# Optimization experiments

Hardware: AMD Instinct MI355X
Metric: run time of the kernel (lower is better)

The kernel has to match this reference:

```python
import jax, jax.numpy as jnp
import numpy as np

N = 100000   # nodes
E = 1600000  # edges (avg degree 16)
D = 64       # input feature dim


def _lin(k, i, o):
    return (jax.random.normal(k, (i, o), jnp.float32) / np.float32(np.sqrt(i)))


def setup_inputs() -> dict:
    key = jax.random.key(0)
    ks = jax.random.split(key, 12)
    return {
        "x": jax.random.normal(ks[0], (N, D), jnp.float32),
        "edge_index": jax.random.randint(ks[1], (2, E), 0, N, dtype=jnp.int64),
        # layer 1: SAGEConv(64, 64, 'pool')
        "W1_pool": _lin(ks[2], 64, 64), "b1_pool": jnp.zeros((64,), jnp.float32),
        "W1_self": _lin(ks[3], 64, 64), "W1_neigh": _lin(ks[4], 64, 64),
        "b1": jnp.zeros((64,), jnp.float32),
        # layer 2: SAGEConv(64, 32, 'pool')
        "W2_pool": _lin(ks[5], 64, 64), "b2_pool": jnp.zeros((64,), jnp.float32),
        "W2_self": _lin(ks[6], 64, 32), "W2_neigh": _lin(ks[7], 64, 32),
        "b2": jnp.zeros((32,), jnp.float32),
        # layer 3: SAGEConv(32, 32, 'mean')
        "W3_self": _lin(ks[8], 32, 32), "W3_neigh": _lin(ks[9], 32, 32),
        "b3": jnp.zeros((32,), jnp.float32),
    }


def _sage_pool(x, src, dst, Wp, bp, Ws, Wn, b):
    # max-pool aggregator: transform all nodes once (cheaper than per-edge),
    # gather per-edge, segment-max into destination nodes.
    m = jax.nn.relu(x @ Wp + bp)[src]                      # [E, in]
    agg = jax.ops.segment_max(m, dst, num_segments=N)     # [N, in]
    agg = jnp.where(jnp.isfinite(agg), agg, jnp.float32(0.0))  # isolated nodes -> 0
    return x @ Ws + agg @ Wn + b


def _sage_mean(x, src, dst, Ws, Wn, b):
    s = jax.ops.segment_sum(x[src], dst, num_segments=N)   # [N, in]
    cnt = jax.ops.segment_sum(jnp.ones((src.shape[0],), jnp.float32), dst,
                              num_segments=N)
    agg = s / jnp.maximum(cnt, jnp.float32(1.0))[:, None]
    return x @ Ws + agg @ Wn + b


def reference(x, edge_index,
              W1_pool, b1_pool, W1_self, W1_neigh, b1,
              W2_pool, b2_pool, W2_self, W2_neigh, b2,
              W3_self, W3_neigh, b3):
    src, dst = edge_index[0], edge_index[1]
    h = jax.nn.relu(_sage_pool(x, src, dst, W1_pool, b1_pool, W1_self, W1_neigh, b1))
    h = _sage_pool(h, src, dst, W2_pool, b2_pool, W2_self, W2_neigh, b2)
    h = _sage_mean(h, src, dst, W3_self, W3_neigh, b3)
    return h
```

## Files before the change

### kernel.cpp

```cpp
#include <hip/hip_runtime.h>
#include <hip/hip_bf16.h>


typedef unsigned int uint;
typedef short short8 __attribute__((ext_vector_type(8)));
typedef float f32x4 __attribute__((ext_vector_type(4)));
typedef float f32x2 __attribute__((ext_vector_type(2)));
typedef unsigned short u16x8 __attribute__((ext_vector_type(8)));

__device__ __forceinline__ float bf2f(unsigned short h){
  return __uint_as_float(((uint)h) << 16);
}
__device__ __forceinline__ unsigned short f2bf(float f){
  uint u = __float_as_uint(f);
  u += 0x7fffu + ((u >> 16) & 1u);
  return (unsigned short)(u >> 16);
}
__device__ __forceinline__ float lo16(uint u){ return __uint_as_float(u << 16); }
__device__ __forceinline__ float hi16(uint u){ return __uint_as_float(u & 0xffff0000u); }

__device__ __forceinline__ uint4 pkmax4(uint4 a, uint4 b){
  u16x8 x = __builtin_bit_cast(u16x8, a);
  u16x8 y = __builtin_bit_cast(u16x8, b);
  return __builtin_bit_cast(uint4, __builtin_elementwise_max(x, y));
}
__device__ __forceinline__ uint4 shflx4(uint4 a, int off){
  uint4 r;
  r.x = (uint)__shfl_xor((int)a.x, off, 64);
  r.y = (uint)__shfl_xor((int)a.y, off, 64);
  r.z = (uint)__shfl_xor((int)a.z, off, 64);
  r.w = (uint)__shfl_xor((int)a.w, off, 64);
  return r;
}
__device__ __forceinline__ f32x2 b2lo(uint u){
  f32x2 r; r.x = lo16(u); r.y = hi16(u); return r;
}

struct WConv {
  const void* src[13];
  int n[13], isbias[13], Cs[13], K[13], off[13];
};

__global__ void conv_w(WConv wc, unsigned short* wtbase, float* bbase,
                       const unsigned short* x, const int* ei,
                       int* flags, int* ccur, int NB){
  __shared__ int sflags[2];
  int t = threadIdx.x;
  if (t < 64){
    int sane = 0;
    #pragma unroll
    for (int k = 0; k < 4; ++k){
      int e = (x[(t * 4 + k) * 2] >> 7) & 0xff;
      sane += (e >= 118 && e <= 134);
    }
    #pragma unroll
    for (int off = 32; off; off >>= 1) sane += __shfl_down(sane, off, 64);
    unsigned long long b = __ballot(ei[1 + 2 * t] != 0);
    if (t == 0){ sflags[0] = (sane >= 128); sflags[1] = (b == 0ull); }
  }
  __syncthreads();
  int isbf = sflags[0];
  if (blockIdx.x == 0){
    if (t == 0){ flags[0] = sflags[0]; flags[1] = sflags[1]; }
    for (int i = t; i < NB; i += 256) ccur[i] = 0;
  }
  int bt = blockIdx.x, n = wc.n[bt];
  if (wc.isbias[bt]){
    float* d = bbase + wc.off[bt];
    for (int i = t; i < n; i += 256)
      d[i] = isbf ? bf2f(((const unsigned short*)wc.src[bt])[i])
                  : ((const float*)wc.src[bt])[i];
  } else {
    unsigned short* d = wtbase + wc.off[bt];
    int Cs = wc.Cs[bt], K = wc.K[bt], Cm = (1 << Cs) - 1;
    for (int i = t; i < n; i += 256){
      int k = i >> Cs, c = i & Cm;
      unsigned short v = isbf ? ((const unsigned short*)wc.src[bt])[i]
                              : f2bf(((const float*)wc.src[bt])[i]);
      d[c * K + k] = v;
    }
  }
}

__device__ __forceinline__ void load_edge(const void* ei, int E, int is64, int e,
                                          int& s, int& d){
  if (is64){
    const long long* p = (const long long*)ei;
    s = (int)p[e]; d = (int)p[E + e];
  } else {
    const int* p = (const int*)ei;
    s = p[e]; d = p[E + e];
  }
}

#define CSR_CE 8192

__global__ __launch_bounds__(256) void csr_phase1(
    const void* __restrict__ ei, const int* __restrict__ flags,
    int* __restrict__ ccur, uint* __restrict__ pairs,
    int E, int N, int NB, int S, int CAP)
{
  __shared__ uint hist[1024];
  __shared__ uint gbase[1024];
  int is64 = flags[1];
  int t = threadIdx.x;
  uint dmask = (1u << S) - 1u;
  int e0 = blockIdx.x * CSR_CE;
  for (int i = t; i < 1024; i += 256) hist[i] = 0;
  __syncthreads();
  #pragma unroll 4
  for (int it = 0; it < CSR_CE / 256; ++it){
    int e = e0 + it * 256 + t;
    if (e >= E) break;
    int s, d; load_edge(ei, E, is64, e, s, d);
    if ((unsigned)s >= (unsigned)N || (unsigned)d >= (unsigned)N) continue;
    atomicAdd(&hist[d >> S], 1u);
  }
  __syncthreads();
  for (int b = t; b < NB; b += 256){
    uint c = hist[b];
    if (c) gbase[b] = (uint)atomicAdd(&ccur[b], (int)c);
    hist[b] = 0;
  }
  __syncthreads();
  #pragma unroll 4
  for (int it = 0; it < CSR_CE / 256; ++it){
    int e = e0 + it * 256 + t;
    if (e >= E) break;
    int s, d; load_edge(ei, E, is64, e, s, d);
    if ((unsigned)s >= (unsigned)N || (unsigned)d >= (unsigned)N) continue;
    int b = d >> S;
    uint local = atomicAdd(&hist[b], 1u);
    uint pos = gbase[b] + local;
    if (pos >= (uint)CAP) pos = (uint)CAP - 1;
    pairs[(size_t)b * CAP + pos] = ((uint)s << S) | ((uint)d & dmask);
  }
}

__global__ void csr_scan0(const int* __restrict__ ccur, int* __restrict__ cbase,
                          int* __restrict__ rowptrN, int NB, int CAP)
{
  __shared__ int sm[256];
  int t = threadIdx.x;
  int g = (NB + 255) / 256;
  int vb = t * g, v[4], s = 0;
  for (int k = 0; k < g; ++k){
    int i = vb + k; int x = (i < NB) ? min(ccur[i], CAP) : 0; v[k] = x; s += x;
  }
  sm[t] = s; __syncthreads();
  for (int off = 1; off < 256; off <<= 1){
    int x = (t >= off) ? sm[t - off] : 0;
    __syncthreads(); sm[t] += x; __syncthreads();
  }
  int run = sm[t] - s;
  for (int k = 0; k < g; ++k){
    int i = vb + k;
    if (i < NB){ cbase[i] = run; run += v[k]; }
  }
  if (t == 255){ cbase[NB] = run; *rowptrN = run; }
}

#define P2_CAP 6144
__global__ __launch_bounds__(256) void csr_phase2(
    const int* __restrict__ cbase, const int* __restrict__ ccur,
    const uint* __restrict__ pairs,
    int* __restrict__ bucket, int* __restrict__ row_ptr, int N, int S, int CAP)
{
  __shared__ int lbuf[P2_CAP];
  __shared__ int cur[1024];
  __shared__ int sm[256];
  int b = blockIdx.x, t = threadIdx.x;
  uint dmask = (1u << S) - 1u;
  int n0 = b << S;
  int n1 = n0 + (1 << S); if (n1 > N) n1 = N;
  int nn = n1 - n0;
  int base = cbase[b];
  int cnt = min(ccur[b], CAP);
  const uint* bp = pairs + (size_t)b * CAP;

  for (int i = t; i < nn; i += 256) cur[i] = 0;
  __syncthreads();
  for (int j = t; j < cnt; j += 256)
    atomicAdd(&cur[(int)(bp[j] & dmask)], 1);
  __syncthreads();
  int g = (nn + 255) / 256, vb = t * g, v[4], s = 0;
  for (int k = 0; k < g; ++k){
    int i = vb + k; int x = (i < nn) ? cur[i] : 0; v[k] = x; s += x;
  }
  sm[t] = s; __syncthreads();
  for (int off = 1; off < 256; off <<= 1){
    int x = (t >= off) ? sm[t - off] : 0;
    __syncthreads(); sm[t] += x; __syncthreads();
  }
  int run = sm[t] - s;
  for (int k = 0; k < g; ++k){
    int i = vb + k;
    if (i < nn){ row_ptr[n0 + i] = base + run; cur[i] = run; run += v[k]; }
  }
  __syncthreads();
  if (cnt <= 0) return;
  if (cnt <= P2_CAP){
    for (int j = t; j < cnt; j += 256){
      uint pr = bp[j];
      int pos = atomicAdd(&cur[(int)(pr & dmask)], 1);
      lbuf[pos] = (int)(pr >> S);
    }
    __syncthreads();
    for (int i = t; i < cnt; i += 256) bucket[base + i] = lbuf[i];
  } else {
    for (int j = t; j < cnt; j += 256){
      uint pr = bp[j];
      int pos = atomicAdd(&cur[(int)(pr & dmask)], 1);
      bucket[base + pos] = (int)(pr >> S);
    }
  }
}

__global__ __launch_bounds__(256) void gather_max64(
    const int* __restrict__ row_ptr, const int* __restrict__ bucket,
    const unsigned short* __restrict__ m, unsigned short* __restrict__ agg, int N)
{
  int wave = (int)((blockIdx.x * 256u + threadIdx.x) >> 6);
  int lane = threadIdx.x & 63;
  int nodeA = wave * 2, nodeB = nodeA + 1;
  if (nodeA >= N) return;
  bool hasB = nodeB < N;
  int rsA = row_ptr[nodeA], reA = row_ptr[nodeA + 1];
  int cntA = reA - rsA;
  int rsB = reA, cntB = hasB ? (row_ptr[nodeB + 1] - reA) : 0;
  int fg8 = (lane & 7) * 8, rowsel = lane >> 3;
  uint4 accA = {0u,0u,0u,0u}, accB = {0u,0u,0u,0u};
  int cmax = max(cntA, cntB);
  for (int c0 = 0; c0 < cmax; c0 += 64){
    int chA = min(cntA - c0, 64);
    int chB = min(cntB - c0, 64);
    int bvA = (lane < chA) ? bucket[rsA + c0 + lane] : 0;
    int bvB = (lane < chB) ? bucket[rsB + c0 + lane] : 0;
    int it = (max(chA, chB) + 7) >> 3;
    for (int k = 0; k < it; ++k){
      int j = k * 8 + rowsel;
      int sA = __shfl(bvA, j, 64);
      int sB = __shfl(bvB, j, 64);
      uint4 vA = *(const uint4*)(m + (size_t)sA * 64 + fg8);
      uint4 vB = *(const uint4*)(m + (size_t)sB * 64 + fg8);
      if (j < chA) accA = pkmax4(accA, vA);
      if (j < chB) accB = pkmax4(accB, vB);
    }
  }
  #pragma unroll
  for (int off = 8; off <= 32; off <<= 1){
    accA = pkmax4(accA, shflx4(accA, off));
    accB = pkmax4(accB, shflx4(accB, off));
  }
  if (lane < 8){
    *(uint4*)(agg + (size_t)nodeA * 64 + fg8) = accA;
  } else if (lane < 16 && hasB){
    *(uint4*)(agg + (size_t)nodeB * 64 + (lane & 7) * 8) = accB;
  }
}

__device__ __forceinline__ short8 ld_fragA_bf16(const unsigned short* A, int row,
                                                int K, int koff){
  return *(const short8*)(A + (size_t)row * K + koff);
}
__device__ __forceinline__ short8 ld_fragA_f32(const float* A, int row,
                                               int K, int koff){
  const float* q = A + (size_t)row * K + koff;
  float4 f0 = *(const float4*)q;
  float4 f1 = *(const float4*)(q + 4);
  short8 r;
  r[0] = (short)f2bf(f0.x); r[1] = (short)f2bf(f0.y);
  r[2] = (short)f2bf(f0.z); r[3] = (short)f2bf(f0.w);
  r[4] = (short)f2bf(f1.x); r[5] = (short)f2bf(f1.y);
  r[6] = (short)f2bf(f1.z); r[7] = (short)f2bf(f1.w);
  return r;
}
__device__ __forceinline__ unsigned short f2bf_relu(float f){
  return (unsigned short)(f2bf(fmaxf(f, 0.f)) & 0x7fff);
}

template<int KA, int KB, int CT, bool RELU, bool OUTF32, int AMODE>
__global__ __launch_bounds__(256) void mfma_mm(
    const void* __restrict__ Av, const unsigned short* __restrict__ Bv,
    const unsigned short* __restrict__ WaT, const unsigned short* __restrict__ WbT,
    const float* __restrict__ bias,
    const int* __restrict__ flags, void* __restrict__ outv, int N)
{
  constexpr int C = CT * 16;
  int wid = threadIdx.x >> 6, lane = threadIdx.x & 63;
  int g = blockIdx.x * 4 + wid;
  int rt, ct;
  if constexpr (CT == 4){ rt = g >> 2; ct = g & 3; }
  else                  { rt = g >> 1; ct = g & 1; }
  int RT = (N + 15) >> 4;
  if (rt >= RT) return;
  int m = lane & 15, quad = lane >> 4;
  int row = rt * 16 + m;
  int rowc = row < N ? row : N - 1;
  int colbase = ct * 16;
  int koq = quad * 8;

  bool af32 = (AMODE == 2) && (flags[0] == 0);
  f32x4 accS = {0.f, 0.f, 0.f, 0.f};

  #pragma unroll
  for (int k0 = 0; k0 < KA; k0 += 32){
    short8 af = af32 ? ld_fragA_f32((const float*)Av, rowc, KA, k0 + koq)
                     : ld_fragA_bf16((const unsigned short*)Av, rowc, KA, k0 + koq);
    short8 wf = *(const short8*)(WaT + (size_t)(colbase + m) * KA + k0 + koq);
    accS = __builtin_amdgcn_mfma_f32_16x16x32_bf16(af, wf, accS, 0, 0, 0);
  }
  if constexpr (KB > 0){
    #pragma unroll
    for (int k0 = 0; k0 < KB; k0 += 32){
      short8 bf = ld_fragA_bf16(Bv, rowc, KB, k0 + koq);
      short8 wf = *(const short8*)(WbT + (size_t)(colbase + m) * KB + k0 + koq);
      accS = __builtin_amdgcn_mfma_f32_16x16x32_bf16(bf, wf, accS, 0, 0, 0);
    }
  }
  float bv = bias[colbase + m];
  #pragma unroll
  for (int r = 0; r < 4; ++r){
    int orow = rt * 16 + quad * 4 + r;
    if (orow >= N) continue;
    float v = accS[r] + bv;
    if constexpr (OUTF32){
      if constexpr (RELU) v = fmaxf(v, 0.f);
      ((float*)outv)[(size_t)orow * C + colbase + m] = v;
    } else {
      unsigned short o;
      if constexpr (RELU) o = f2bf_relu(v);
      else                o = f2bf(v);
      ((unsigned short*)outv)[(size_t)orow * C + colbase + m] = o;
    }
  }
}

template<int AMODE>
__global__ __launch_bounds__(256) void mfma_mm_fused(
    const void* __restrict__ Av, const unsigned short* __restrict__ Bv,
    const unsigned short* __restrict__ WaT, const unsigned short* __restrict__ WbT,
    const float* __restrict__ bias1,
    const unsigned short* __restrict__ WcT, const float* __restrict__ bias2,
    const int* __restrict__ flags,
    unsigned short* __restrict__ out1, unsigned short* __restrict__ out2, int N)
{
  constexpr int K = 64, C = 64, LDH = 72;
  __shared__ unsigned short hl[16 * LDH];
  int wid = threadIdx.x >> 6, lane = threadIdx.x & 63;
  int rt = blockIdx.x;
  int m = lane & 15, quad = lane >> 4;
  int row = rt * 16 + m;
  int rowc = row < N ? row : N - 1;
  int colbase = wid * 16;
  int koq = quad * 8;
  bool af32 = (AMODE == 2) && (flags[0] == 0);

  f32x4 acc = {0.f, 0.f, 0.f, 0.f};
  #pragma unroll
  for (int k0 = 0; k0 < K; k0 += 32){
    short8 af = af32 ? ld_fragA_f32((const float*)Av, rowc, K, k0 + koq)
                     : ld_fragA_bf16((const unsigned short*)Av, rowc, K, k0 + koq);
    short8 wf = *(const short8*)(WaT + (size_t)(colbase + m) * K + k0 + koq);
    acc = __builtin_amdgcn_mfma_f32_16x16x32_bf16(af, wf, acc, 0, 0, 0);
    short8 bf = ld_fragA_bf16(Bv, rowc, K, k0 + koq);
    short8 wg = *(const short8*)(WbT + (size_t)(colbase + m) * K + k0 + koq);
    acc = __builtin_amdgcn_mfma_f32_16x16x32_bf16(bf, wg, acc, 0, 0, 0);
  }
  float bv = bias1[colbase + m];
  #pragma unroll
  for (int r = 0; r < 4; ++r){
    int rl = quad * 4 + r;
    int orow = rt * 16 + rl;
    unsigned short hb = f2bf_relu(acc[r] + bv);
    hl[rl * LDH + colbase + m] = hb;
    if (orow < N) out1[(size_t)orow * C + colbase + m] = hb;
  }
  __syncthreads();
  f32x4 acc2 = {0.f, 0.f, 0.f, 0.f};
  #pragma unroll
  for (int k0 = 0; k0 < K; k0 += 32){
    short8 af = *(const short8*)(hl + m * LDH + k0 + koq);
    short8 wf = *(const short8*)(WcT + (size_t)(colbase + m) * K + k0 + koq);
    acc2 = __builtin_amdgcn_mfma_f32_16x16x32_bf16(af, wf, acc2, 0, 0, 0);
  }
  float b2v = bias2[colbase + m];
  #pragma unroll
  for (int r = 0; r < 4; ++r){
    int orow = rt * 16 + quad * 4 + r;
    if (orow < N)
      out2[(size_t)orow * C + colbase + m] = f2bf_relu(acc2[r] + b2v);
  }
}

__global__ __launch_bounds__(256) void gsum3(
    const int* __restrict__ row_ptr, const int* __restrict__ bucket,
    const unsigned short* __restrict__ h2,
    const unsigned short* __restrict__ W3sT, const unsigned short* __restrict__ W3nT,
    const float* __restrict__ b3, float* __restrict__ out, int N)
{
  constexpr int LDA = 40;
  __shared__ unsigned short la[16 * LDA];
  int t = threadIdx.x;
  int w = t >> 6, lane = t & 63;
  int n0 = blockIdx.x * 16;
  int g = lane >> 4, q = lane & 15;
  int nd = n0 + w * 4 + g;
  int ndc = nd < N ? nd : N - 1;
  int rs = row_ptr[ndc];
  int cnt = (nd < N) ? (row_ptr[ndc + 1] - rs) : 0;
  int fg8 = (q & 3) * 8, rowsel = q >> 2;
  f32x2 a0 = {0.f,0.f}, a1 = {0.f,0.f}, a2 = {0.f,0.f}, a3 = {0.f,0.f};
  for (int c0 = 0; c0 < cnt; c0 += 16){
    int chunk = min(cnt - c0, 16);
    int bval = (q < chunk) ? bucket[rs + c0 + q] : 0;
    int it = (chunk + 3) >> 2;
    for (int k = 0; k < it; ++k){
      int j = k * 4 + rowsel;
      int s = __shfl(bval, (g << 4) + j, 64);
      uint4 v = *(const uint4*)(h2 + (size_t)s * 32 + fg8);
      if (j < chunk){
        a0 += b2lo(v.x); a1 += b2lo(v.y); a2 += b2lo(v.z); a3 += b2lo(v.w);
      }
    }
  }
  #pragma unroll
  for (int off = 4; off <= 8; off <<= 1){
    a0.x += __shfl_xor(a0.x, off, 64); a0.y += __shfl_xor(a0.y, off, 64);
    a1.x += __shfl_xor(a1.x, off, 64); a1.y += __shfl_xor(a1.y, off, 64);
    a2.x += __shfl_xor(a2.x, off, 64); a2.y += __shfl_xor(a2.y, off, 64);
    a3.x += __shfl_xor(a3.x, off, 64); a3.y += __shfl_xor(a3.y, off, 64);
  }
  if (rowsel == 0){
    float sc = 1.f / fmaxf((float)cnt, 1.f);
    int r = w * 4 + g;
    uint4 pk;
    pk.x = (uint)f2bf(a0.x * sc) | ((uint)f2bf(a0.y * sc) << 16);
    pk.y = (uint)f2bf(a1.x * sc) | ((uint)f2bf(a1.y * sc) << 16);
    pk.z = (uint)f2bf(a2.x * sc) | ((uint)f2bf(a2.y * sc) << 16);
    pk.w = (uint)f2bf(a3.x * sc) | ((uint)f2bf(a3.y * sc) << 16);
    *(uint4*)(la + r * LDA + q * 8) = pk;
  }
  __syncthreads();
  if (w < 2){
    int m = lane & 15, quad = lane >> 4, koq = quad * 8;
    int colbase = w * 16;
    int row = n0 + m;
    int rowc = row < N ? row : N - 1;
    f32x4 acc = {0.f, 0.f, 0.f, 0.f};
    short8 aself = *(const short8*)(h2 + (size_t)rowc * 32 + koq);
    short8 wfs = *(const short8*)(W3sT + (size_t)(colbase + m) * 32 + koq);
    acc = __builtin_amdgcn_mfma_f32_16x16x32_bf16(aself, wfs, acc, 0, 0, 0);
    short8 aagg = *(const short8*)(la + m * LDA + koq);
    short8 wfn = *(const short8*)(W3nT + (size_t)(colbase + m) * 32 + koq);
    acc = __builtin_amdgcn_mfma_f32_16x16x32_bf16(aagg, wfn, acc, 0, 0, 0);
    float bv = b3[colbase + m];
    #pragma unroll
    for (int r = 0; r < 4; ++r){
      int orow = n0 + quad * 4 + r;
      if (orow < N) out[(size_t)orow * 32 + colbase + m] = acc[r] + bv;
    }
  }
}

static inline char* align256(char* p){
  return (char*)(((uintptr_t)p + 255) & ~(uintptr_t)255);
}

extern "C" void kernel_launch(void* const* d_in, const int* in_sizes, int n_in,
                              void* d_out, int out_size, void* d_ws, size_t ws_size,
                              hipStream_t stream)
{
  const void* x = d_in[0];
  const void* ei = d_in[1];
  int N = in_sizes[0] / 64;
  int E = in_sizes[1] / 2;

  char* ws = (char*)d_ws;
  unsigned short* wtbase = (unsigned short*)ws;
  float* bbase = (float*)(ws + 65536);
  int* flags = (int*)(ws + 131072 - 256);

  int S = 7, NB = (N + 127) >> 7;
  while (NB > 1024){ S++; NB = (N + (1 << S) - 1) >> S; }
  int CAP = ((2 * E / NB) + 255) & ~255;
  if (CAP < 1024) CAP = 1024;

  char* p = ws + 131072;
  int* row_ptr = (int*)p; p = align256(p + (size_t)(N + 1) * 4);
  int* cbase   = (int*)p; p = align256(p + 4352);
  int* ccur    = (int*)p; p = align256(p + 4352);
  int* bucket  = (int*)p; p = align256(p + (size_t)E * 4);
  uint* pairs  = (uint*)p; p = align256(p + (size_t)NB * CAP * 4);
  char* P = p;  p = align256(p + (size_t)N * 64 * 2);
  char* Q = p;  p = align256(p + (size_t)N * 64 * 2);
  char* R = p;  p = align256(p + (size_t)N * 64 * 2);
  unsigned short* mbuf = (unsigned short*)P;
  unsigned short* h2   = (unsigned short*)P;
  unsigned short* aggb = (unsigned short*)Q;
  unsigned short* h1   = (unsigned short*)R;

  WConv wc;
  {
    const int widx[13] = {2, 3, 4, 5, 6, 7, 8, 9, 10, 11, 12, 13, 14};
    const int isb[13]  = {0, 1, 0, 0, 1, 0, 1, 0, 0, 1, 0, 0, 1};
    const int Cs[13]   = {6, 0, 6, 6, 0, 6, 0, 5, 5, 0, 5, 5, 0};
    const int Kk[13]   = {64, 0, 64, 64, 0, 64, 0, 64, 64, 0, 32, 32, 0};
    const int off[13]  = {0, 0, 4096, 8192, 64, 12288, 128, 16384, 18432, 192,
                          20480, 21504, 224};
    for (int i = 0; i < 13; ++i){
      wc.src[i] = d_in[widx[i]]; wc.n[i] = in_sizes[widx[i]];
      wc.isbias[i] = isb[i]; wc.Cs[i] = Cs[i]; wc.K[i] = Kk[i]; wc.off[i] = off[i];
    }
  }
  hipLaunchKernelGGL(conv_w, dim3(13), dim3(256), 0, stream, wc, wtbase, bbase,
                     (const unsigned short*)x, (const int*)ei, flags, ccur, NB);
  unsigned short* W1pT = wtbase + 0;     unsigned short* W1sT = wtbase + 4096;
  unsigned short* W1nT = wtbase + 8192;  unsigned short* W2pT = wtbase + 12288;
  unsigned short* W2sT = wtbase + 16384; unsigned short* W2nT = wtbase + 18432;
  unsigned short* W3sT = wtbase + 20480; unsigned short* W3nT = wtbase + 21504;
  float* b1p = bbase + 0;  float* b1 = bbase + 64; float* b2p = bbase + 128;
  float* b2 = bbase + 192; float* b3 = bbase + 224;

  int nP = (E + CSR_CE - 1) / CSR_CE;
  csr_phase1<<<nP, 256, 0, stream>>>(ei, flags, ccur, pairs, E, N, NB, S, CAP);
  csr_scan0<<<1, 256, 0, stream>>>(ccur, cbase, row_ptr + N, NB, CAP);
  csr_phase2<<<NB, 256, 0, stream>>>(cbase, ccur, pairs, bucket, row_ptr, N, S, CAP);

  int RT = (N + 15) / 16;
  int gc2 = (RT * 2 + 3) / 4;
  int gg = (N + 7) / 8;

  mfma_mm<64,0,4,true,false,2><<<RT,256,0,stream>>>(
      x, nullptr, W1pT, nullptr, b1p, flags, mbuf, N);
  gather_max64<<<gg,256,0,stream>>>(row_ptr, bucket, mbuf, aggb, N);
  mfma_mm_fused<2><<<RT,256,0,stream>>>(
      x, aggb, W1sT, W1nT, b1, W2pT, b2p, flags, h1, mbuf, N);

  gather_max64<<<gg,256,0,stream>>>(row_ptr, bucket, mbuf, aggb, N);
  mfma_mm<64,64,2,false,false,0><<<gc2,256,0,stream>>>(
      h1, aggb, W2sT, W2nT, b2, flags, h2, N);

  gsum3<<<RT,256,0,stream>>>(row_ptr, bucket, h2, W3sT, W3nT, b3,
                             (float*)d_out, N);
}
```

Before: 307.5 us.

## Fuse CSR phase1 with layer-1 pool matmul and widen matmul row tiles

Merges the CSR histogram/scatter pass and the layer-1 pool projection into one launch, with block ranges split by role, so the two independent jobs overlap and one launch is saved. Phase1 now caches edge loads in registers instead of reading the edge list twice, and its chunk size shrinks so there are more blocks. The fused and layer-2 matmuls each process 32 rows per wave so every weight fragment is reused across two MFMAs. The cost is more register pressure and a heterogeneous kernel whose LDS allocation is sized for the CSR path.

```diff
diff --git a/kernel.cpp b/kernel.cpp
--- a/kernel.cpp
+++ b/kernel.cpp
@@ -93,28 +93,52 @@
   }
 }
 
-#define CSR_CE 8192
-
-__global__ __launch_bounds__(256) void csr_phase1(
+__device__ __forceinline__ short8 ld_fragA_bf16(const unsigned short* A, int row,
+                                                int K, int koff){
+  return *(const short8*)(A + (size_t)row * K + koff);
+}
+__device__ __forceinline__ short8 ld_fragA_f32(const float* A, int row,
+                                               int K, int koff){
+  const float* q = A + (size_t)row * K + koff;
+  float4 f0 = *(const float4*)q;
+  float4 f1 = *(const float4*)(q + 4);
+  short8 r;
+  r[0] = (short)f2bf(f0.x); r[1] = (short)f2bf(f0.y);
+  r[2] = (short)f2bf(f0.z); r[3] = (short)f2bf(f0.w);
+  r[4] = (short)f2bf(f1.x); r[5] = (short)f2bf(f1.y);
+  r[6] = (short)f2bf(f1.z); r[7] = (short)f2bf(f1.w);
+  return r;
+}
+__device__ __forceinline__ unsigned short f2bf_relu(float f){
+  return (unsigned short)(f2bf(fmaxf(f, 0.f)) & 0x7fff);
+}
+
+#define CSR_CE 2048
+
+__device__ __forceinline__ void phase1_body(
     const void* __restrict__ ei, const int* __restrict__ flags,
     int* __restrict__ ccur, uint* __restrict__ pairs,
-    int E, int N, int NB, int S, int CAP)
-{
-  __shared__ uint hist[1024];
-  __shared__ uint gbase[1024];
-  int is64 = flags[1];
+    int E, int N, int NB, int S, int CAP, int blk,
+    uint* hist, uint* gbase)
+{
   int t = threadIdx.x;
   uint dmask = (1u << S) - 1u;
-  int e0 = blockIdx.x * CSR_CE;
+  int is64 = flags[1];
+  int e0 = blk * CSR_CE;
   for (int i = t; i < 1024; i += 256) hist[i] = 0;
   __syncthreads();
-  #pragma unroll 4
-  for (int it = 0; it < CSR_CE / 256; ++it){
-    int e = e0 + it * 256 + t;
-    if (e >= E) break;
-    int s, d; load_edge(ei, E, is64, e, s, d);
-    if ((unsigned)s >= (unsigned)N || (unsigned)d >= (unsigned)N) continue;
-    atomicAdd(&hist[d >> S], 1u);
+  uint pr[8]; short bb[8];
+  #pragma unroll
+  for (int k = 0; k < 8; ++k){
+    int e = e0 + k * 256 + t;
+    int s = 0, d = 0; bool ok = (e < E);
+    if (ok){
+      load_edge(ei, E, is64, e, s, d);
+      ok = (unsigned)s < (unsigned)N && (unsigned)d < (unsigned)N;
+    }
+    bb[k] = ok ? (short)(d >> S) : (short)(-1);
+    pr[k] = ((uint)s << S) | ((uint)d & dmask);
+    if (ok) atomicAdd(&hist[d >> S], 1u);
   }
   __syncthreads();
   for (int b = t; b < NB; b += 256){
@@ -123,18 +147,67 @@
     hist[b] = 0;
   }
   __syncthreads();
-  #pragma unroll 4
-  for (int it = 0; it < CSR_CE / 256; ++it){
-    int e = e0 + it * 256 + t;
-    if (e >= E) break;
-    int s, d; load_edge(ei, E, is64, e, s, d);
-    if ((unsigned)s >= (unsigned)N || (unsigned)d >= (unsigned)N) continue;
-    int b = d >> S;
-    uint local = atomicAdd(&hist[b], 1u);
-    uint pos = gbase[b] + local;
-    if (pos >= (uint)CAP) pos = (uint)CAP - 1;
-    pairs[(size_t)b * CAP + pos] = ((uint)s << S) | ((uint)d & dmask);
-  }
+  #pragma unroll
+  for (int k = 0; k < 8; ++k){
+    int b = (int)bb[k];
+    if (b >= 0){
+      uint local = atomicAdd(&hist[b], 1u);
+      uint pos = gbase[b] + local;
+      if (pos >= (uint)CAP) pos = (uint)CAP - 1;
+      pairs[(size_t)b * CAP + pos] = pr[k];
+    }
+  }
+}
+
+template<int AMODE>
+__device__ __forceinline__ void mm1_body(
+    const void* __restrict__ Av, const unsigned short* __restrict__ WaT,
+    const float* __restrict__ bias, const int* __restrict__ flags,
+    unsigned short* __restrict__ out, int N, int blk)
+{
+  int wid = threadIdx.x >> 6, lane = threadIdx.x & 63;
+  int n0 = blk * 32;
+  int m = lane & 15, quad = lane >> 4, koq = quad * 8;
+  int colbase = wid * 16;
+  int rowc0 = min(n0 + m, N - 1);
+  int rowc1 = min(n0 + 16 + m, N - 1);
+  bool af32 = (AMODE == 2) && (flags[0] == 0);
+  f32x4 a0 = {0.f,0.f,0.f,0.f}, a1 = {0.f,0.f,0.f,0.f};
+  #pragma unroll
+  for (int k0 = 0; k0 < 64; k0 += 32){
+    short8 af0 = af32 ? ld_fragA_f32((const float*)Av, rowc0, 64, k0 + koq)
+                      : ld_fragA_bf16((const unsigned short*)Av, rowc0, 64, k0 + koq);
+    short8 af1 = af32 ? ld_fragA_f32((const float*)Av, rowc1, 64, k0 + koq)
+                      : ld_fragA_bf16((const unsigned short*)Av, rowc1, 64, k0 + koq);
+    short8 wf = *(const short8*)(WaT + (size_t)(colbase + m) * 64 + k0 + koq);
+    a0 = __builtin_amdgcn_mfma_f32_16x16x32_bf16(af0, wf, a0, 0, 0, 0);
+    a1 = __builtin_amdgcn_mfma_f32_16x16x32_bf16(af1, wf, a1, 0, 0, 0);
+  }
+  float bv = bias[colbase + m];
+  #pragma unroll
+  for (int r = 0; r < 4; ++r){
+    int rl = quad * 4 + r;
+    if (n0 + rl < N)
+      out[(size_t)(n0 + rl) * 64 + colbase + m] = f2bf_relu(a0[r] + bv);
+    if (n0 + 16 + rl < N)
+      out[(size_t)(n0 + 16 + rl) * 64 + colbase + m] = f2bf_relu(a1[r] + bv);
+  }
+}
+
+template<int AMODE>
+__global__ __launch_bounds__(256) void phase1_mm1(
+    const void* __restrict__ ei, const int* __restrict__ flags,
+    int* __restrict__ ccur, uint* __restrict__ pairs,
+    int E, int N, int NB, int S, int CAP, int nP,
+    const void* __restrict__ x, const unsigned short* __restrict__ W1pT,
+    const float* __restrict__ b1p, unsigned short* __restrict__ mbuf)
+{
+  __shared__ uint hist[1024];
+  __shared__ uint gbase[1024];
+  if ((int)blockIdx.x < nP)
+    phase1_body(ei, flags, ccur, pairs, E, N, NB, S, CAP, blockIdx.x, hist, gbase);
+  else
+    mm1_body<AMODE>(x, W1pT, b1p, flags, mbuf, N, blockIdx.x - nP);
 }
 
 __global__ void csr_scan0(const int* __restrict__ ccur, int* __restrict__ cbase,
@@ -259,83 +332,6 @@
   }
 }
 
-__device__ __forceinline__ short8 ld_fragA_bf16(const unsigned short* A, int row,
-                                                int K, int koff){
-  return *(const short8*)(A + (size_t)row * K + koff);
-}
-__device__ __forceinline__ short8 ld_fragA_f32(const float* A, int row,
-                                               int K, int koff){
-  const float* q = A + (size_t)row * K + koff;
-  float4 f0 = *(const float4*)q;
-  float4 f1 = *(const float4*)(q + 4);
-  short8 r;
-  r[0] = (short)f2bf(f0.x); r[1] = (short)f2bf(f0.y);
-  r[2] = (short)f2bf(f0.z); r[3] = (short)f2bf(f0.w);
-  r[4] = (short)f2bf(f1.x); r[5] = (short)f2bf(f1.y);
-  r[6] = (short)f2bf(f1.z); r[7] = (short)f2bf(f1.w);
-  return r;
-}
-__device__ __forceinline__ unsigned short f2bf_relu(float f){
-  return (unsigned short)(f2bf(fmaxf(f, 0.f)) & 0x7fff);
-}
-
-template<int KA, int KB, int CT, bool RELU, bool OUTF32, int AMODE>
-__global__ __launch_bounds__(256) void mfma_mm(
-    const void* __restrict__ Av, const unsigned short* __restrict__ Bv,
-    const unsigned short* __restrict__ WaT, const unsigned short* __restrict__ WbT,
-    const float* __restrict__ bias,
-    const int* __restrict__ flags, void* __restrict__ outv, int N)
-{
-  constexpr int C = CT * 16;
-  int wid = threadIdx.x >> 6, lane = threadIdx.x & 63;
-  int g = blockIdx.x * 4 + wid;
-  int rt, ct;
-  if constexpr (CT == 4){ rt = g >> 2; ct = g & 3; }
-  else                  { rt = g >> 1; ct = g & 1; }
-  int RT = (N + 15) >> 4;
-  if (rt >= RT) return;
-  int m = lane & 15, quad = lane >> 4;
-  int row = rt * 16 + m;
-  int rowc = row < N ? row : N - 1;
-  int colbase = ct * 16;
-  int koq = quad * 8;
-
-  bool af32 = (AMODE == 2) && (flags[0] == 0);
-  f32x4 accS = {0.f, 0.f, 0.f, 0.f};
-
-  #pragma unroll
-  for (int k0 = 0; k0 < KA; k0 += 32){
-    short8 af = af32 ? ld_fragA_f32((const float*)Av, rowc, KA, k0 + koq)
-                     : ld_fragA_bf16((const unsigned short*)Av, rowc, KA, k0 + koq);
-    short8 wf = *(const short8*)(WaT + (size_t)(colbase + m) * KA + k0 + koq);
-    accS = __builtin_amdgcn_mfma_f32_16x16x32_bf16(af, wf, accS, 0, 0, 0);
-  }
-  if constexpr (KB > 0){
-    #pragma unroll
-    for (int k0 = 0; k0 < KB; k0 += 32){
-      short8 bf = ld_fragA_bf16(Bv, rowc, KB, k0 + koq);
-      short8 wf = *(const short8*)(WbT + (size_t)(colbase + m) * KB + k0 + koq);
-      accS = __builtin_amdgcn_mfma_f32_16x16x32_bf16(bf, wf, accS, 0, 0, 0);
-    }
-  }
-  float bv = bias[colbase + m];
-  #pragma unroll
-  for (int r = 0; r < 4; ++r){
-    int orow = rt * 16 + quad * 4 + r;
-    if (orow >= N) continue;
-    float v = accS[r] + bv;
-    if constexpr (OUTF32){
-      if constexpr (RELU) v = fmaxf(v, 0.f);
-      ((float*)outv)[(size_t)orow * C + colbase + m] = v;
-    } else {
-      unsigned short o;
-      if constexpr (RELU) o = f2bf_relu(v);
-      else                o = f2bf(v);
-      ((unsigned short*)outv)[(size_t)orow * C + colbase + m] = o;
-    }
-  }
-}
-
 template<int AMODE>
 __global__ __launch_bounds__(256) void mfma_mm_fused(
     const void* __restrict__ Av, const unsigned short* __restrict__ Bv,
@@ -346,50 +342,95 @@
     unsigned short* __restrict__ out1, unsigned short* __restrict__ out2, int N)
 {
   constexpr int K = 64, C = 64, LDH = 72;
-  __shared__ unsigned short hl[16 * LDH];
+  __shared__ unsigned short hl[32 * LDH];
   int wid = threadIdx.x >> 6, lane = threadIdx.x & 63;
-  int rt = blockIdx.x;
-  int m = lane & 15, quad = lane >> 4;
-  int row = rt * 16 + m;
-  int rowc = row < N ? row : N - 1;
+  int n0 = blockIdx.x * 32;
+  int m = lane & 15, quad = lane >> 4, koq = quad * 8;
   int colbase = wid * 16;
-  int koq = quad * 8;
+  int rowc0 = min(n0 + m, N - 1);
+  int rowc1 = min(n0 + 16 + m, N - 1);
   bool af32 = (AMODE == 2) && (flags[0] == 0);
 
-  f32x4 acc = {0.f, 0.f, 0.f, 0.f};
+  f32x4 a0 = {0.f,0.f,0.f,0.f}, a1 = {0.f,0.f,0.f,0.f};
   #pragma unroll
   for (int k0 = 0; k0 < K; k0 += 32){
-    short8 af = af32 ? ld_fragA_f32((const float*)Av, rowc, K, k0 + koq)
-                     : ld_fragA_bf16((const unsigned short*)Av, rowc, K, k0 + koq);
+    short8 af0 = af32 ? ld_fragA_f32((const float*)Av, rowc0, K, k0 + koq)
+                      : ld_fragA_bf16((const unsigned short*)Av, rowc0, K, k0 + koq);
+    short8 af1 = af32 ? ld_fragA_f32((const float*)Av, rowc1, K, k0 + koq)
+                      : ld_fragA_bf16((const unsigned short*)Av, rowc1, K, k0 + koq);
     short8 wf = *(const short8*)(WaT + (size_t)(colbase + m) * K + k0 + koq);
-    acc = __builtin_amdgcn_mfma_f32_16x16x32_bf16(af, wf, acc, 0, 0, 0);
-    short8 bf = ld_fragA_bf16(Bv, rowc, K, k0 + koq);
+    a0 = __builtin_amdgcn_mfma_f32_16x16x32_bf16(af0, wf, a0, 0, 0, 0);
+    a1 = __builtin_amdgcn_mfma_f32_16x16x32_bf16(af1, wf, a1, 0, 0, 0);
+    short8 bf0 = ld_fragA_bf16(Bv, rowc0, K, k0 + koq);
+    short8 bf1 = ld_fragA_bf16(Bv, rowc1, K, k0 + koq);
     short8 wg = *(const short8*)(WbT + (size_t)(colbase + m) * K + k0 + koq);
-    acc = __builtin_amdgcn_mfma_f32_16x16x32_bf16(bf, wg, acc, 0, 0, 0);
+    a0 = __builtin_amdgcn_mfma_f32_16x16x32_bf16(bf0, wg, a0, 0, 0, 0);
+    a1 = __builtin_amdgcn_mfma_f32_16x16x32_bf16(bf1, wg, a1, 0, 0, 0);
   }
   float bv = bias1[colbase + m];
   #pragma unroll
   for (int r = 0; r < 4; ++r){
     int rl = quad * 4 + r;
-    int orow = rt * 16 + rl;
-    unsigned short hb = f2bf_relu(acc[r] + bv);
-    hl[rl * LDH + colbase + m] = hb;
-    if (orow < N) out1[(size_t)orow * C + colbase + m] = hb;
-  }
-  __syncthreads();
-  f32x4 acc2 = {0.f, 0.f, 0.f, 0.f};
+    unsigned short h0 = f2bf_relu(a0[r] + bv);
+    unsigned short h1v = f2bf_relu(a1[r] + bv);
+    hl[rl * LDH + colbase + m] = h0;
+    hl[(16 + rl) * LDH + colbase + m] = h1v;
+    if (n0 + rl < N) out1[(size_t)(n0 + rl) * C + colbase + m] = h0;
+    if (n0 + 16 + rl < N) out1[(size_t)(n0 + 16 + rl) * C + colbase + m] = h1v;
+  }
+  __syncthreads();
+  f32x4 c0 = {0.f,0.f,0.f,0.f}, c1 = {0.f,0.f,0.f,0.f};
   #pragma unroll
   for (int k0 = 0; k0 < K; k0 += 32){
-    short8 af = *(const short8*)(hl + m * LDH + k0 + koq);
+    short8 q0 = *(const short8*)(hl + m * LDH + k0 + koq);
+    short8 q1 = *(const short8*)(hl + (16 + m) * LDH + k0 + koq);
     short8 wf = *(const short8*)(WcT + (size_t)(colbase + m) * K + k0 + koq);
-    acc2 = __builtin_amdgcn_mfma_f32_16x16x32_bf16(af, wf, acc2, 0, 0, 0);
+    c0 = __builtin_amdgcn_mfma_f32_16x16x32_bf16(q0, wf, c0, 0, 0, 0);
+    c1 = __builtin_amdgcn_mfma_f32_16x16x32_bf16(q1, wf, c1, 0, 0, 0);
   }
   float b2v = bias2[colbase + m];
   #pragma unroll
   for (int r = 0; r < 4; ++r){
-    int orow = rt * 16 + quad * 4 + r;
-    if (orow < N)
-      out2[(size_t)orow * C + colbase + m] = f2bf_relu(acc2[r] + b2v);
+    int rl = quad * 4 + r;
+    if (n0 + rl < N)
+      out2[(size_t)(n0 + rl) * C + colbase + m] = f2bf_relu(c0[r] + b2v);
+    if (n0 + 16 + rl < N)
+      out2[(size_t)(n0 + 16 + rl) * C + colbase + m] = f2bf_relu(c1[r] + b2v);
+  }
+}
+
+__global__ __launch_bounds__(256) void mfma_mm2(
+    const unsigned short* __restrict__ h1, const unsigned short* __restrict__ aggb,
+    const unsigned short* __restrict__ WsT, const unsigned short* __restrict__ WnT,
+    const float* __restrict__ bias, unsigned short* __restrict__ h2, int N)
+{
+  int wid = threadIdx.x >> 6, lane = threadIdx.x & 63;
+  int n0 = blockIdx.x * 64 + (wid >> 1) * 32;
+  int colbase = (wid & 1) * 16;
+  int m = lane & 15, quad = lane >> 4, koq = quad * 8;
+  int rowc0 = min(n0 + m, N - 1), rowc1 = min(n0 + 16 + m, N - 1);
+  f32x4 a0 = {0.f,0.f,0.f,0.f}, a1 = {0.f,0.f,0.f,0.f};
+  #pragma unroll
+  for (int k0 = 0; k0 < 64; k0 += 32){
+    short8 af0 = *(const short8*)(h1 + (size_t)rowc0 * 64 + k0 + koq);
+    short8 af1 = *(const short8*)(h1 + (size_t)rowc1 * 64 + k0 + koq);
+    short8 wf = *(const short8*)(WsT + (size_t)(colbase + m) * 64 + k0 + koq);
+    a0 = __builtin_amdgcn_mfma_f32_16x16x32_bf16(af0, wf, a0, 0, 0, 0);
+    a1 = __builtin_amdgcn_mfma_f32_16x16x32_bf16(af1, wf, a1, 0, 0, 0);
+    short8 bf0 = *(const short8*)(aggb + (size_t)rowc0 * 64 + k0 + koq);
+    short8 bf1 = *(const short8*)(aggb + (size_t)rowc1 * 64 + k0 + koq);
+    short8 wg = *(const short8*)(WnT + (size_t)(colbase + m) * 64 + k0 + koq);
+    a0 = __builtin_amdgcn_mfma_f32_16x16x32_bf16(bf0, wg, a0, 0, 0, 0);
+    a1 = __builtin_amdgcn_mfma_f32_16x16x32_bf16(bf1, wg, a1, 0, 0, 0);
+  }
+  float bv = bias[colbase + m];
+  #pragma unroll
+  for (int r = 0; r < 4; ++r){
+    int rl = quad * 4 + r;
+    if (n0 + rl < N)
+      h2[(size_t)(n0 + rl) * 32 + colbase + m] = f2bf(a0[r] + bv);
+    if (n0 + 16 + rl < N)
+      h2[(size_t)(n0 + 16 + rl) * 32 + colbase + m] = f2bf(a1[r] + bv);
   }
 }
 
@@ -523,24 +564,22 @@
   float* b2 = bbase + 192; float* b3 = bbase + 224;
 
   int nP = (E + CSR_CE - 1) / CSR_CE;
-  csr_phase1<<<nP, 256, 0, stream>>>(ei, flags, ccur, pairs, E, N, NB, S, CAP);
+  int RT32 = (N + 31) / 32;
+  int RT16 = (N + 15) / 16;
+  int gg = (N + 7) / 8;
+
+  phase1_mm1<2><<<nP + RT32, 256, 0, stream>>>(
+      ei, flags, ccur, pairs, E, N, NB, S, CAP, nP, x, W1pT, b1p, mbuf);
   csr_scan0<<<1, 256, 0, stream>>>(ccur, cbase, row_ptr + N, NB, CAP);
   csr_phase2<<<NB, 256, 0, stream>>>(cbase, ccur, pairs, bucket, row_ptr, N, S, CAP);
 
-  int RT = (N + 15) / 16;
-  int gc2 = (RT * 2 + 3) / 4;
-  int gg = (N + 7) / 8;
-
-  mfma_mm<64,0,4,true,false,2><<<RT,256,0,stream>>>(
-      x, nullptr, W1pT, nullptr, b1p, flags, mbuf, N);
   gather_max64<<<gg,256,0,stream>>>(row_ptr, bucket, mbuf, aggb, N);
-  mfma_mm_fused<2><<<RT,256,0,stream>>>(
+  mfma_mm_fused<2><<<RT32,256,0,stream>>>(
       x, aggb, W1sT, W1nT, b1, W2pT, b2p, flags, h1, mbuf, N);
 
   gather_max64<<<gg,256,0,stream>>>(row_ptr, bucket, mbuf, aggb, N);
-  mfma_mm<64,64,2,false,false,0><<<gc2,256,0,stream>>>(
-      h1, aggb, W2sT, W2nT, b2, flags, h2, N);
-
-  gsum3<<<RT,256,0,stream>>>(row_ptr, bucket, h2, W3sT, W3nT, b3,
-                             (float*)d_out, N);
-}
+  mfma_mm2<<<(N + 63) / 64,256,0,stream>>>(h1, aggb, W2sT, W2nT, b2, h2, N);
+
+  gsum3<<<RT16,256,0,stream>>>(row_ptr, bucket, h2, W3sT, W3nT, b3,
+                               (float*)d_out, N);
+}
```

After: 292.3 us. -4.9%, faster.
